# Kernel optimization log

Hardware: AMD Instinct MI355X
Metric: run time of the kernel (lower is better)

The kernel has to match this reference:

```python
import jax, jax.numpy as jnp
import numpy as np

DECOHERENCE = 0.01   # NoiseModel(decoherence_rate=0.01)
DEPOL = 0.01         # depolarization_rate
MEAS_ERR = 0.01      # measurement_error_rate
EPS = 1e-12


def _normalize(x):
    # L2-normalize quantum state amplitudes along the last axis
    return x / (jnp.linalg.norm(x, axis=-1, keepdims=True) + EPS)


def setup_inputs() -> dict:
    V, B, S, Q, depth = 32000, 2, 2048, 4, 2
    dim = 2 ** Q  # 16
    key = jax.random.key(0)
    k1, k2, k3 = jax.random.split(key, 3)
    input_ids = jax.random.randint(k1, (B, S), 0, V)
    attention_mask = jnp.ones((B, S), dtype=jnp.int32)
    # embedding table: one_hot @ W_embed == embedding lookup
    W_embed = 0.02 * jax.random.normal(k2, (V, dim), dtype=jnp.float32)
    # per-layer 16x16 unitary gates (orthogonal via QR)
    rng = np.random.default_rng(0)
    gates = np.stack([np.linalg.qr(rng.standard_normal((dim, dim)))[0] for _ in range(depth)])
    gates = jnp.asarray(gates.astype(np.float32))  # [depth, dim, dim]
    # output projection Linear(dim, V)
    W_out = 0.02 * jax.random.normal(k3, (V, dim), dtype=jnp.float32)
    b_out = jnp.zeros((V,), dtype=jnp.float32)
    return dict(input_ids=input_ids, attention_mask=attention_mask,
                W_embed=W_embed, gates=gates, W_out=W_out, b_out=b_out)


def reference(input_ids, attention_mask, W_embed, gates, W_out, b_out):
    V = W_embed.shape[0]
    # F.one_hot(input_ids, vocab).float() then quantum embed (project + normalize)
    onehot = jax.nn.one_hot(input_ids, V, dtype=W_embed.dtype)        # [B,S,V]
    emb = _normalize(onehot @ W_embed)                                # [B,S,16]
    dim = emb.shape[-1]
    # Vectorized noisy quantum circuit applied to every token at once
    state = emb
    for l in range(gates.shape[0]):
        state = jnp.einsum('bsd,ed->bse', state, gates[l])            # gate unitary
        state = state * (1.0 - DECOHERENCE)                           # decoherence damping
        state = (1.0 - DEPOL) * state + DEPOL / dim                   # depolarization mix
        state = _normalize(state)
    state = (1.0 - MEAS_ERR) * state + MEAS_ERR / dim                 # measurement error
    # per-position gate: circuit applied only if mask[:, i] is all True
    apply = jnp.all(attention_mask.astype(bool), axis=0)              # [S]
    processed = jnp.where(apply[None, :, None], state, emb)           # [B,S,16]
    return processed @ W_out.T + b_out                                # [B,S,V]
```

## Files before the change

kernel.cpp:

```cpp
#include <hip/hip_runtime.h>
#include <math.h>

#define DIM 16
#define BATCH 2
#define TT 16

__global__ void quantum_state_kernel(const int* __restrict__ ids,
                                     const int* __restrict__ mask,
                                     const float* __restrict__ W_embed,
                                     const float* __restrict__ gates,
                                     float* __restrict__ proc,
                                     int B, int S, int depth) {
    extern __shared__ float g[];
    const int tid = threadIdx.x;
    const int ng = depth * DIM * DIM;
    for (int i = tid; i < ng; i += blockDim.x) g[i] = gates[i];
    __syncthreads();

    const int t = blockIdx.x * blockDim.x + tid;
    const int total = B * S;
    if (t >= total) return;
    const int s_idx = t % S;

    const int id = ids[t];
    const float* row = W_embed + (long)id * DIM;
    float e[DIM];
    float ss = 0.f;
#pragma unroll
    for (int k = 0; k < DIM; ++k) { e[k] = row[k]; ss += e[k] * e[k]; }
    float inv = 1.0f / (sqrtf(ss) + 1e-12f);
#pragma unroll
    for (int k = 0; k < DIM; ++k) e[k] *= inv;

    float st[DIM];
#pragma unroll
    for (int k = 0; k < DIM; ++k) st[k] = e[k];
    for (int l = 0; l < depth; ++l) {
        const float* gl = g + l * DIM * DIM;
        float ns[DIM];
#pragma unroll
        for (int ei = 0; ei < DIM; ++ei) {
            float acc = 0.f;
#pragma unroll
            for (int d = 0; d < DIM; ++d) acc += gl[ei * DIM + d] * st[d];
            ns[ei] = acc;
        }
        ss = 0.f;
#pragma unroll
        for (int k = 0; k < DIM; ++k) {
            float v = ns[k] * 0.99f;
            v = 0.99f * v + 0.000625f;
            ns[k] = v;
            ss += v * v;
        }
        inv = 1.0f / (sqrtf(ss) + 1e-12f);
#pragma unroll
        for (int k = 0; k < DIM; ++k) st[k] = ns[k] * inv;
    }
#pragma unroll
    for (int k = 0; k < DIM; ++k) st[k] = 0.99f * st[k] + 0.000625f;

    bool apply = true;
    for (int b = 0; b < B; ++b) apply = apply && (mask[b * S + s_idx] != 0);

#pragma unroll
    for (int k = 0; k < DIM; ++k) proc[(long)t * DIM + k] = apply ? st[k] : e[k];
}

__global__ __launch_bounds__(256) void out_proj_kernel(
        const float* __restrict__ proc,
        const float* __restrict__ W_out,
        const float* __restrict__ b_out,
        float* __restrict__ out,
        int V, int total_tokens) {
    __shared__ float sstate[TT][DIM];
    const int tid = threadIdx.x;
    const int t0 = blockIdx.x * TT;

    {
        const int tok = tid >> 4;
        const int k   = tid & 15;
        const int t   = t0 + tok;
        sstate[tok][k] = (t < total_tokens) ? proc[(long)t * DIM + k] : 0.f;
    }
    __syncthreads();

    const int v0 = blockIdx.y * 1024 + tid * 4;
    if (v0 >= V) return;

    float w[4][DIM];
#pragma unroll
    for (int j = 0; j < 4; ++j) {
        const float4* wr = (const float4*)(W_out + (long)(v0 + j) * DIM);
        const float4 a = wr[0], b4 = wr[1], c = wr[2], d = wr[3];
        w[j][0]  = a.x;  w[j][1]  = a.y;  w[j][2]  = a.z;  w[j][3]  = a.w;
        w[j][4]  = b4.x; w[j][5]  = b4.y; w[j][6]  = b4.z; w[j][7]  = b4.w;
        w[j][8]  = c.x;  w[j][9]  = c.y;  w[j][10] = c.z;  w[j][11] = c.w;
        w[j][12] = d.x;  w[j][13] = d.y;  w[j][14] = d.z;  w[j][15] = d.w;
    }
    const float4 bias = *(const float4*)(b_out + v0);

#pragma unroll
    for (int tk = 0; tk < TT; ++tk) {
        const int t = t0 + tk;
        if (t < total_tokens) {
            const float4* sp = (const float4*)sstate[tk];
            const float4 s0 = sp[0], s1 = sp[1], s2 = sp[2], s3 = sp[3];
            const float sv[DIM] = {s0.x, s0.y, s0.z, s0.w,
                                   s1.x, s1.y, s1.z, s1.w,
                                   s2.x, s2.y, s2.z, s2.w,
                                   s3.x, s3.y, s3.z, s3.w};
            float a0 = bias.x, a1 = bias.y, a2 = bias.z, a3 = bias.w;
#pragma unroll
            for (int k = 0; k < DIM; ++k) {
                a0 = fmaf(sv[k], w[0][k], a0);
                a1 = fmaf(sv[k], w[1][k], a1);
                a2 = fmaf(sv[k], w[2][k], a2);
                a3 = fmaf(sv[k], w[3][k], a3);
            }
            *(float4*)(out + (long)t * V + v0) = make_float4(a0, a1, a2, a3);
        }
    }
}

extern "C" void kernel_launch(void* const* d_in, const int* in_sizes, int n_in,
                              void* d_out, int out_size, void* d_ws, size_t ws_size,
                              hipStream_t stream) {
    const int*   ids    = (const int*)  d_in[0];
    const int*   mask   = (const int*)  d_in[1];
    const float* W_emb  = (const float*)d_in[2];
    const float* gates  = (const float*)d_in[3];
    const float* W_out  = (const float*)d_in[4];
    const float* b_out  = (const float*)d_in[5];
    float* out = (float*)d_out;

    const int B = BATCH;
    const int total = in_sizes[0];
    const int S = total / B;
    const int V = in_sizes[5];
    const int depth = in_sizes[3] / (DIM * DIM);

    float* proc = (float*)d_ws;

    {
        dim3 block(64);
        dim3 grid((total + 63) / 64);
        size_t shmem = (size_t)depth * DIM * DIM * sizeof(float);
        quantum_state_kernel<<<grid, block, shmem, stream>>>(
            ids, mask, W_emb, gates, proc, B, S, depth);
    }

    {
        dim3 block(256);
        dim3 grid((total + TT - 1) / TT, (V + 1023) / 1024);
        out_proj_kernel<<<grid, block, 0, stream>>>(proc, W_out, b_out, out, V, total);
    }
}
```

Before: 626.1 us.

## Use nontemporal stores, direct state loads, and larger token tiles in output projection

The output projection kernel now writes logits with nontemporal stores, reads each token's state vector straight from global memory with a uniform 64-byte load instead of staging it through shared memory, and processes 32 tokens per block instead of 16. The state kernel uses 16-wide vector loads and stores. The aim is to cut cache pollution on the large write-bound output and remove the shared-memory sync. The cost is partial unrolling and repeated global state loads, which rely on cache hits.

```diff
diff --git a/kernel.cpp b/kernel.cpp
--- a/kernel.cpp
+++ b/kernel.cpp
@@ -3,7 +3,10 @@
 
 #define DIM 16
 #define BATCH 2
-#define TT 16
+#define TT 32
+
+typedef float f32x4  __attribute__((ext_vector_type(4)));
+typedef float f32x16 __attribute__((ext_vector_type(16)));
 
 __global__ void quantum_state_kernel(const int* __restrict__ ids,
                                      const int* __restrict__ mask,
@@ -23,21 +26,18 @@
     const int s_idx = t % S;
 
     const int id = ids[t];
-    const float* row = W_embed + (long)id * DIM;
-    float e[DIM];
+    f32x16 e = *(const f32x16*)(W_embed + (size_t)id * DIM);
     float ss = 0.f;
 #pragma unroll
-    for (int k = 0; k < DIM; ++k) { e[k] = row[k]; ss += e[k] * e[k]; }
+    for (int k = 0; k < DIM; ++k) ss += e[k] * e[k];
     float inv = 1.0f / (sqrtf(ss) + 1e-12f);
 #pragma unroll
     for (int k = 0; k < DIM; ++k) e[k] *= inv;
 
-    float st[DIM];
-#pragma unroll
-    for (int k = 0; k < DIM; ++k) st[k] = e[k];
+    f32x16 st = e;
     for (int l = 0; l < depth; ++l) {
         const float* gl = g + l * DIM * DIM;
-        float ns[DIM];
+        f32x16 ns;
 #pragma unroll
         for (int ei = 0; ei < DIM; ++ei) {
             float acc = 0.f;
@@ -63,8 +63,7 @@
     bool apply = true;
     for (int b = 0; b < B; ++b) apply = apply && (mask[b * S + s_idx] != 0);
 
-#pragma unroll
-    for (int k = 0; k < DIM; ++k) proc[(long)t * DIM + k] = apply ? st[k] : e[k];
+    *(f32x16*)(proc + (size_t)t * DIM) = apply ? st : e;
 }
 
 __global__ __launch_bounds__(256) void out_proj_kernel(
@@ -73,53 +72,32 @@
         const float* __restrict__ b_out,
         float* __restrict__ out,
         int V, int total_tokens) {
-    __shared__ float sstate[TT][DIM];
     const int tid = threadIdx.x;
     const int t0 = blockIdx.x * TT;
-
-    {
-        const int tok = tid >> 4;
-        const int k   = tid & 15;
-        const int t   = t0 + tok;
-        sstate[tok][k] = (t < total_tokens) ? proc[(long)t * DIM + k] : 0.f;
-    }
-    __syncthreads();
-
     const int v0 = blockIdx.y * 1024 + tid * 4;
     if (v0 >= V) return;
 
-    float w[4][DIM];
-#pragma unroll
-    for (int j = 0; j < 4; ++j) {
-        const float4* wr = (const float4*)(W_out + (long)(v0 + j) * DIM);
-        const float4 a = wr[0], b4 = wr[1], c = wr[2], d = wr[3];
-        w[j][0]  = a.x;  w[j][1]  = a.y;  w[j][2]  = a.z;  w[j][3]  = a.w;
-        w[j][4]  = b4.x; w[j][5]  = b4.y; w[j][6]  = b4.z; w[j][7]  = b4.w;
-        w[j][8]  = c.x;  w[j][9]  = c.y;  w[j][10] = c.z;  w[j][11] = c.w;
-        w[j][12] = d.x;  w[j][13] = d.y;  w[j][14] = d.z;  w[j][15] = d.w;
-    }
-    const float4 bias = *(const float4*)(b_out + v0);
+    const f32x16 w0 = *(const f32x16*)(W_out + (size_t)(v0 + 0) * DIM);
+    const f32x16 w1 = *(const f32x16*)(W_out + (size_t)(v0 + 1) * DIM);
+    const f32x16 w2 = *(const f32x16*)(W_out + (size_t)(v0 + 2) * DIM);
+    const f32x16 w3 = *(const f32x16*)(W_out + (size_t)(v0 + 3) * DIM);
+    const f32x4 bias = *(const f32x4*)(b_out + v0);
 
-#pragma unroll
+#pragma unroll 2
     for (int tk = 0; tk < TT; ++tk) {
         const int t = t0 + tk;
-        if (t < total_tokens) {
-            const float4* sp = (const float4*)sstate[tk];
-            const float4 s0 = sp[0], s1 = sp[1], s2 = sp[2], s3 = sp[3];
-            const float sv[DIM] = {s0.x, s0.y, s0.z, s0.w,
-                                   s1.x, s1.y, s1.z, s1.w,
-                                   s2.x, s2.y, s2.z, s2.w,
-                                   s3.x, s3.y, s3.z, s3.w};
-            float a0 = bias.x, a1 = bias.y, a2 = bias.z, a3 = bias.w;
+        if (t >= total_tokens) break;
+        const f32x16 sv = *(const f32x16*)(proc + (size_t)t * DIM);
+        float a0 = bias[0], a1 = bias[1], a2 = bias[2], a3 = bias[3];
 #pragma unroll
-            for (int k = 0; k < DIM; ++k) {
-                a0 = fmaf(sv[k], w[0][k], a0);
-                a1 = fmaf(sv[k], w[1][k], a1);
-                a2 = fmaf(sv[k], w[2][k], a2);
-                a3 = fmaf(sv[k], w[3][k], a3);
-            }
-            *(float4*)(out + (long)t * V + v0) = make_float4(a0, a1, a2, a3);
+        for (int k = 0; k < DIM; ++k) {
+            a0 = fmaf(sv[k], w0[k], a0);
+            a1 = fmaf(sv[k], w1[k], a1);
+            a2 = fmaf(sv[k], w2[k], a2);
+            a3 = fmaf(sv[k], w3[k], a3);
         }
+        f32x4 r; r[0] = a0; r[1] = a1; r[2] = a2; r[3] = a3;
+        __builtin_nontemporal_store(r, (f32x4*)(out + (size_t)t * V + v0));
     }
 }
 
```

Measured after the change: 548.2 us. 12.4% less time.
